# Kernel tuning notes

Measured on AMD Instinct MI355X. Metric: run time of the kernel, lower is better.

The kernel has to match this reference:

```python
import jax, jax.numpy as jnp
import numpy as np

B, T, I, H, O = 512, 1024, 15, 64, 11

def setup_inputs() -> dict:
    key = jax.random.key(0)
    ks = jax.random.split(key, 7)
    s_ih = 1.0 / np.sqrt(H)
    return {
        "x": jax.random.normal(ks[0], (B, T, I), dtype=jnp.float32),
        # torch nn.RNN params: weight_ih_l0 [H,I], weight_hh_l0 [H,H], biases [H]
        "W_ih": jax.random.uniform(ks[1], (H, I), jnp.float32, -s_ih, s_ih),
        "b_ih": jax.random.uniform(ks[2], (H,), jnp.float32, -s_ih, s_ih),
        "W_hh": jax.random.uniform(ks[3], (H, H), jnp.float32, -s_ih, s_ih),
        "b_hh": jax.random.uniform(ks[4], (H,), jnp.float32, -s_ih, s_ih),
        # decoder Linear(64, 11)
        "W_dec": jax.random.uniform(ks[5], (O, H), jnp.float32, -s_ih, s_ih),
        "b_dec": jax.random.uniform(ks[6], (O,), jnp.float32, -s_ih, s_ih),
    }

def reference(x, W_ih, b_ih, W_hh, b_hh, W_dec, b_dec):
    # Precompute input projection for all timesteps: [T, B, H]
    xproj = jnp.einsum("bti,hi->tbh", x, W_ih) + b_ih + b_hh
    h0 = jnp.zeros((x.shape[0], W_hh.shape[0]), dtype=x.dtype)

    def step(h, xp_t):
        h_new = jax.nn.relu(xp_t + h @ W_hh.T)  # [B, H]
        return h_new, h_new

    h_last, hs = jax.lax.scan(step, h0, xproj)  # hs: [T, B, H]
    out_seq = jnp.transpose(hs, (1, 0, 2))       # [B, T, H]
    out = jax.nn.relu(jnp.einsum("bth,oh->bto", out_seq, W_dec) + b_dec)
    h = h_last[None]  # [1, B, H] matching torch num_layers dim
    return (out, h)
```

## Files before the change

kernel.cpp:

```cpp
#include <hip/hip_runtime.h>
#include <hip/hip_fp16.h>
#include <stdint.h>

#define BB 512
#define TT 1024
#define II 15
#define HH 64
#define OO 11

typedef __fp16 half2v __attribute__((ext_vector_type(2)));
typedef float floatx4 __attribute__((ext_vector_type(4)));
typedef int int4v __attribute__((ext_vector_type(4)));

union PK { int i; half2v h; float f; };

__device__ __forceinline__ half2v i2h2(int v) { PK u; u.i = v; return u.h; }
__device__ __forceinline__ int h22i(half2v v) { PK u; u.h = v; return u.i; }

__device__ __forceinline__ float FDOT2(half2v a, half2v b, float c) {
    return __builtin_amdgcn_fdot2(a, b, c, false);
}

__device__ __forceinline__ float lane_xor1(float v) {
    PK u; u.f = v;
    u.i = __builtin_amdgcn_mov_dpp(u.i, 0xB1, 0xF, 0xF, false);
    return u.f;
}

__device__ __forceinline__ float lane_xor2(float v) {
    PK u; u.f = v;
    u.i = __builtin_amdgcn_mov_dpp(u.i, 0x4E, 0xF, 0xF, false);
    return u.f;
}

__device__ __forceinline__ void block_sync() {
    asm volatile("s_waitcnt lgkmcnt(0)" ::: "memory");
    __builtin_amdgcn_s_barrier();
}

__global__ __launch_bounds__(256) void rnn_fused(
    const float* __restrict__ x, const float* __restrict__ W_ih,
    const float* __restrict__ b_ih, const float* __restrict__ W_hh,
    const float* __restrict__ b_hh, const float* __restrict__ W_dec,
    const float* __restrict__ b_dec, float* __restrict__ out,
    float* __restrict__ h_last)
{
    __shared__ __align__(16) int xbuf[2][2][64 * 8];
    __shared__ __align__(16) _Float16 hring[2][128][HH];
    const int tid  = threadIdx.x;
    const int lane = tid & 63;
    const int wid  = tid >> 6;

    if (wid < 2) {
        const int w = wid;
        const int b = blockIdx.x * 2 + w;

        half2v whh[32];
#pragma unroll
        for (int p = 0; p < 32; ++p)
            whh[p] = __builtin_amdgcn_cvt_pkrtz(W_hh[lane * HH + 2 * p],
                                                W_hh[lane * HH + 2 * p + 1]);
        half2v wx[8];
#pragma unroll
        for (int j = 0; j < 7; ++j)
            wx[j] = __builtin_amdgcn_cvt_pkrtz(W_ih[lane * II + 2 * j],
                                               W_ih[lane * II + 2 * j + 1]);
        wx[7] = __builtin_amdgcn_cvt_pkrtz(W_ih[lane * II + 14],
                                           b_ih[lane] + b_hh[lane]);

        const float* xb = x + (size_t)b * TT * II;

        {
            float cf[II];
#pragma unroll
            for (int i = 0; i < II; ++i) cf[i] = xb[lane * II + i];
            int4v p0, p1;
            p0.x = h22i(__builtin_amdgcn_cvt_pkrtz(cf[0], cf[1]));
            p0.y = h22i(__builtin_amdgcn_cvt_pkrtz(cf[2], cf[3]));
            p0.z = h22i(__builtin_amdgcn_cvt_pkrtz(cf[4], cf[5]));
            p0.w = h22i(__builtin_amdgcn_cvt_pkrtz(cf[6], cf[7]));
            p1.x = h22i(__builtin_amdgcn_cvt_pkrtz(cf[8], cf[9]));
            p1.y = h22i(__builtin_amdgcn_cvt_pkrtz(cf[10], cf[11]));
            p1.z = h22i(__builtin_amdgcn_cvt_pkrtz(cf[12], cf[13]));
            p1.w = h22i(__builtin_amdgcn_cvt_pkrtz(cf[14], 1.0f));
            *(int4v*)&xbuf[w][0][lane * 8] = p0;
            *(int4v*)&xbuf[w][0][lane * 8 + 4] = p1;
        }
        hring[w][127][lane] = (_Float16)0.0f;

        float xa[8];
        {
            const int4v xv0 = *(const int4v*)&xbuf[w][0][0];
            const int4v xv1 = *(const int4v*)&xbuf[w][0][4];
            xa[0] = FDOT2(i2h2(xv0.x), wx[0], 0.0f);
            xa[1] = FDOT2(i2h2(xv0.y), wx[1], 0.0f);
            xa[2] = FDOT2(i2h2(xv0.z), wx[2], 0.0f);
            xa[3] = FDOT2(i2h2(xv0.w), wx[3], 0.0f);
            xa[4] = FDOT2(i2h2(xv1.x), wx[4], 0.0f);
            xa[5] = FDOT2(i2h2(xv1.y), wx[5], 0.0f);
            xa[6] = FDOT2(i2h2(xv1.z), wx[6], 0.0f);
            xa[7] = FDOT2(i2h2(xv1.w), wx[7], 0.0f);
        }

        float h = 0.0f;
        int hpk = 0;

        auto step = [&](int t) {
            const int4v* hb4 = (const int4v*)&hring[w][(t + 127) & 127][0];
            int4v hb[6];
#pragma unroll
            for (int q = 0; q < 6; ++q) hb[q] = hb4[q + 2];

            float a0 = xa[0], a1 = xa[1], a2 = xa[2], a3 = xa[3];
            float a4 = xa[4], a5 = xa[5], a6 = xa[6], a7 = xa[7];

            a0 = FDOT2(i2h2(__builtin_amdgcn_readlane(hpk, 0)),  whh[0], a0);
            a1 = FDOT2(i2h2(__builtin_amdgcn_readlane(hpk, 2)),  whh[1], a1);
            a2 = FDOT2(i2h2(__builtin_amdgcn_readlane(hpk, 4)),  whh[2], a2);
            a3 = FDOT2(i2h2(__builtin_amdgcn_readlane(hpk, 6)),  whh[3], a3);
            a4 = FDOT2(i2h2(__builtin_amdgcn_readlane(hpk, 8)),  whh[4], a4);
            a5 = FDOT2(i2h2(__builtin_amdgcn_readlane(hpk, 10)), whh[5], a5);
            a6 = FDOT2(i2h2(__builtin_amdgcn_readlane(hpk, 12)), whh[6], a6);
            a7 = FDOT2(i2h2(__builtin_amdgcn_readlane(hpk, 14)), whh[7], a7);

#pragma unroll
            for (int q = 0; q < 6; ++q) {
                const int base = 8 + 4 * q;
                if ((q & 1) == 0) {
                    a0 = FDOT2(i2h2(hb[q].x), whh[base + 0], a0);
                    a1 = FDOT2(i2h2(hb[q].y), whh[base + 1], a1);
                    a2 = FDOT2(i2h2(hb[q].z), whh[base + 2], a2);
                    a3 = FDOT2(i2h2(hb[q].w), whh[base + 3], a3);
                } else {
                    a4 = FDOT2(i2h2(hb[q].x), whh[base + 0], a4);
                    a5 = FDOT2(i2h2(hb[q].y), whh[base + 1], a5);
                    a6 = FDOT2(i2h2(hb[q].z), whh[base + 2], a6);
                    a7 = FDOT2(i2h2(hb[q].w), whh[base + 3], a7);
                }
            }
            h = fmaxf(((a0 + a1) + (a2 + a3)) + ((a4 + a5) + (a6 + a7)), 0.0f);
            const _Float16 hf = (_Float16)h;
            hring[w][t & 127][lane] = hf;

            const int tn = t + 1;
            const int* xp = &xbuf[w][(tn >> 6) & 1][(tn & 63) * 8];
            const int4v xv0 = *(const int4v*)xp;
            const int4v xv1 = *(const int4v*)(xp + 4);

            hpk = h22i(__builtin_amdgcn_cvt_pkrtz(h, lane_xor1(h)));

            xa[0] = FDOT2(i2h2(xv0.x), wx[0], 0.0f);
            xa[1] = FDOT2(i2h2(xv0.y), wx[1], 0.0f);
            xa[2] = FDOT2(i2h2(xv0.z), wx[2], 0.0f);
            xa[3] = FDOT2(i2h2(xv0.w), wx[3], 0.0f);
            xa[4] = FDOT2(i2h2(xv1.x), wx[4], 0.0f);
            xa[5] = FDOT2(i2h2(xv1.y), wx[5], 0.0f);
            xa[6] = FDOT2(i2h2(xv1.z), wx[6], 0.0f);
            xa[7] = FDOT2(i2h2(xv1.w), wx[7], 0.0f);
        };

        for (int tc = 0; tc < TT; tc += 64) {
            const int tnb = (tc + 64 < TT) ? (tc + 64) : tc;
            float nf[II];
#pragma unroll
            for (int i = 0; i < II; ++i)
                nf[i] = xb[(size_t)(tnb + lane) * II + i];

            for (int to = 0; to < 32; to += 8)
#pragma unroll
                for (int u = 0; u < 8; ++u) step(tc + to + u);

            {
                const int cb = ((tc >> 6) + 1) & 1;
                int4v p0, p1;
                p0.x = h22i(__builtin_amdgcn_cvt_pkrtz(nf[0], nf[1]));
                p0.y = h22i(__builtin_amdgcn_cvt_pkrtz(nf[2], nf[3]));
                p0.z = h22i(__builtin_amdgcn_cvt_pkrtz(nf[4], nf[5]));
                p0.w = h22i(__builtin_amdgcn_cvt_pkrtz(nf[6], nf[7]));
                p1.x = h22i(__builtin_amdgcn_cvt_pkrtz(nf[8], nf[9]));
                p1.y = h22i(__builtin_amdgcn_cvt_pkrtz(nf[10], nf[11]));
                p1.z = h22i(__builtin_amdgcn_cvt_pkrtz(nf[12], nf[13]));
                p1.w = h22i(__builtin_amdgcn_cvt_pkrtz(nf[14], 1.0f));
                *(int4v*)&xbuf[w][cb][lane * 8] = p0;
                *(int4v*)&xbuf[w][cb][lane * 8 + 4] = p1;
            }

            for (int to = 32; to < 64; to += 8)
#pragma unroll
                for (int u = 0; u < 8; ++u) step(tc + to + u);

            block_sync();
        }
        h_last[b * HH + lane] = h;
    } else {
        const int w = wid - 2;
        const int b = blockIdx.x * 2 + w;

        const int od = lane >> 2;
        const int oc = (od < OO) ? od : 0;
        const int ks = lane & 3;
        half2v wdec[8];
#pragma unroll
        for (int p = 0; p < 8; ++p)
            wdec[p] = __builtin_amdgcn_cvt_pkrtz(
                W_dec[oc * HH + (ks * 8 + p) * 2],
                W_dec[oc * HH + (ks * 8 + p) * 2 + 1]);
        const float bd = b_dec[oc];
        const bool dostore = (ks == 0) && (od < OO);
        float* outb = out + (size_t)b * TT * OO + od;

        for (int c = 0; c < TT / 64; ++c) {
            block_sync();
#pragma unroll 4
            for (int lt = 0; lt < 64; ++lt) {
                const int t = c * 64 + lt;
                const char* row = (const char*)&hring[w][t & 127][0];
                const int4v d0 = *(const int4v*)(row + ks * 32);
                const int4v d1 = *(const int4v*)(row + ks * 32 + 16);
                float dacc = FDOT2(i2h2(d0.x), wdec[0], 0.0f);
                dacc = FDOT2(i2h2(d0.y), wdec[1], dacc);
                dacc = FDOT2(i2h2(d0.z), wdec[2], dacc);
                dacc = FDOT2(i2h2(d0.w), wdec[3], dacc);
                dacc = FDOT2(i2h2(d1.x), wdec[4], dacc);
                dacc = FDOT2(i2h2(d1.y), wdec[5], dacc);
                dacc = FDOT2(i2h2(d1.z), wdec[6], dacc);
                dacc = FDOT2(i2h2(d1.w), wdec[7], dacc);
                dacc += lane_xor1(dacc);
                dacc += lane_xor2(dacc);
                if (dostore)
                    outb[(size_t)t * OO] = fmaxf(dacc + bd, 0.0f);
            }
        }
    }
}

extern "C" void kernel_launch(void* const* d_in, const int* in_sizes, int n_in,
                              void* d_out, int out_size, void* d_ws, size_t ws_size,
                              hipStream_t stream) {
    const float* x     = (const float*)d_in[0];
    const float* W_ih  = (const float*)d_in[1];
    const float* b_ih  = (const float*)d_in[2];
    const float* W_hh  = (const float*)d_in[3];
    const float* b_hh  = (const float*)d_in[4];
    const float* W_dec = (const float*)d_in[5];
    const float* b_dec = (const float*)d_in[6];

    float* out    = (float*)d_out;
    float* h_last = out + (size_t)BB * TT * OO;

    rnn_fused<<<BB / 2, 256, 0, stream>>>(x, W_ih, b_ih, W_hh, b_hh,
                                          W_dec, b_dec, out, h_last);
}
```

Baseline: 259.1 us.

## Compute recurrent matvec with MFMA 16x16x32 instead of packed dot2

Replaces the per-lane fdot2 chain over W_hh with eight MFMA 16x16x32 f16 instructions. The hidden vector is broadcast as the A operand, W_hh tiles sit as B fragments in registers, and the needed output element is picked per lane with selects. The goal is to shorten the serial per-timestep latency of the 64x64 matvec. In exchange, most of each MFMA computes redundant rows, and MFMA issue latency plus cross-lane selection sit on the critical recurrence path.

```diff
diff --git a/kernel.cpp b/kernel.cpp
--- a/kernel.cpp
+++ b/kernel.cpp
@@ -9,6 +9,7 @@
 #define OO 11
 
 typedef __fp16 half2v __attribute__((ext_vector_type(2)));
+typedef _Float16 half8 __attribute__((ext_vector_type(8)));
 typedef float floatx4 __attribute__((ext_vector_type(4)));
 typedef int int4v __attribute__((ext_vector_type(4)));
 
@@ -55,11 +56,18 @@
         const int w = wid;
         const int b = blockIdx.x * 2 + w;
 
-        half2v whh[32];
-#pragma unroll
-        for (int p = 0; p < 32; ++p)
-            whh[p] = __builtin_amdgcn_cvt_pkrtz(W_hh[lane * HH + 2 * p],
-                                                W_hh[lane * HH + 2 * p + 1]);
+        const int nl = lane & 15;
+        const int kq = lane >> 4;
+        half8 bf[4][2];
+#pragma unroll
+        for (int g = 0; g < 4; ++g)
+#pragma unroll
+            for (int s = 0; s < 2; ++s)
+#pragma unroll
+                for (int j = 0; j < 8; ++j)
+                    bf[g][s][j] = (_Float16)W_hh[(16 * g + nl) * HH +
+                                                 32 * s + 8 * kq + j];
+
         half2v wx[8];
 #pragma unroll
         for (int j = 0; j < 7; ++j)
@@ -103,51 +111,43 @@
         }
 
         float h = 0.0f;
-        int hpk = 0;
+        const int aoff = kq * 16;
+        const bool b4 = (lane & 16) != 0;
+        const bool b5 = (lane & 32) != 0;
+        const floatx4 zc = {0.0f, 0.0f, 0.0f, 0.0f};
 
         auto step = [&](int t) {
-            const int4v* hb4 = (const int4v*)&hring[w][(t + 127) & 127][0];
-            int4v hb[6];
-#pragma unroll
-            for (int q = 0; q < 6; ++q) hb[q] = hb4[q + 2];
-
-            float a0 = xa[0], a1 = xa[1], a2 = xa[2], a3 = xa[3];
-            float a4 = xa[4], a5 = xa[5], a6 = xa[6], a7 = xa[7];
-
-            a0 = FDOT2(i2h2(__builtin_amdgcn_readlane(hpk, 0)),  whh[0], a0);
-            a1 = FDOT2(i2h2(__builtin_amdgcn_readlane(hpk, 2)),  whh[1], a1);
-            a2 = FDOT2(i2h2(__builtin_amdgcn_readlane(hpk, 4)),  whh[2], a2);
-            a3 = FDOT2(i2h2(__builtin_amdgcn_readlane(hpk, 6)),  whh[3], a3);
-            a4 = FDOT2(i2h2(__builtin_amdgcn_readlane(hpk, 8)),  whh[4], a4);
-            a5 = FDOT2(i2h2(__builtin_amdgcn_readlane(hpk, 10)), whh[5], a5);
-            a6 = FDOT2(i2h2(__builtin_amdgcn_readlane(hpk, 12)), whh[6], a6);
-            a7 = FDOT2(i2h2(__builtin_amdgcn_readlane(hpk, 14)), whh[7], a7);
-
-#pragma unroll
-            for (int q = 0; q < 6; ++q) {
-                const int base = 8 + 4 * q;
-                if ((q & 1) == 0) {
-                    a0 = FDOT2(i2h2(hb[q].x), whh[base + 0], a0);
-                    a1 = FDOT2(i2h2(hb[q].y), whh[base + 1], a1);
-                    a2 = FDOT2(i2h2(hb[q].z), whh[base + 2], a2);
-                    a3 = FDOT2(i2h2(hb[q].w), whh[base + 3], a3);
-                } else {
-                    a4 = FDOT2(i2h2(hb[q].x), whh[base + 0], a4);
-                    a5 = FDOT2(i2h2(hb[q].y), whh[base + 1], a5);
-                    a6 = FDOT2(i2h2(hb[q].z), whh[base + 2], a6);
-                    a7 = FDOT2(i2h2(hb[q].w), whh[base + 3], a7);
-                }
-            }
-            h = fmaxf(((a0 + a1) + (a2 + a3)) + ((a4 + a5) + (a6 + a7)), 0.0f);
-            const _Float16 hf = (_Float16)h;
-            hring[w][t & 127][lane] = hf;
+            const char* hrow = (const char*)&hring[w][(t + 127) & 127][0];
+            const half8 a0 = *(const half8*)(hrow + aoff);
+            const half8 a1 = *(const half8*)(hrow + 64 + aoff);
+
+            const float xs = ((xa[0] + xa[1]) + (xa[2] + xa[3])) +
+                             ((xa[4] + xa[5]) + (xa[6] + xa[7]));
 
             const int tn = t + 1;
             const int* xp = &xbuf[w][(tn >> 6) & 1][(tn & 63) * 8];
             const int4v xv0 = *(const int4v*)xp;
             const int4v xv1 = *(const int4v*)(xp + 4);
 
-            hpk = h22i(__builtin_amdgcn_cvt_pkrtz(h, lane_xor1(h)));
+            floatx4 c0 = __builtin_amdgcn_mfma_f32_16x16x32_f16(a0, bf[0][0], zc, 0, 0, 0);
+            floatx4 d0 = __builtin_amdgcn_mfma_f32_16x16x32_f16(a1, bf[0][1], zc, 0, 0, 0);
+            floatx4 c1 = __builtin_amdgcn_mfma_f32_16x16x32_f16(a0, bf[1][0], zc, 0, 0, 0);
+            floatx4 d1 = __builtin_amdgcn_mfma_f32_16x16x32_f16(a1, bf[1][1], zc, 0, 0, 0);
+            floatx4 c2 = __builtin_amdgcn_mfma_f32_16x16x32_f16(a0, bf[2][0], zc, 0, 0, 0);
+            floatx4 d2 = __builtin_amdgcn_mfma_f32_16x16x32_f16(a1, bf[2][1], zc, 0, 0, 0);
+            floatx4 c3 = __builtin_amdgcn_mfma_f32_16x16x32_f16(a0, bf[3][0], zc, 0, 0, 0);
+            floatx4 d3 = __builtin_amdgcn_mfma_f32_16x16x32_f16(a1, bf[3][1], zc, 0, 0, 0);
+
+            const float v0 = c0[0] + d0[0];
+            const float v1 = c1[0] + d1[0];
+            const float v2 = c2[0] + d2[0];
+            const float v3 = c3[0] + d3[0];
+            const float r01 = b4 ? v1 : v0;
+            const float r23 = b4 ? v3 : v2;
+            const float hpre = b5 ? r23 : r01;
+
+            h = fmaxf(hpre + xs, 0.0f);
+            hring[w][t & 127][lane] = (_Float16)h;
 
             xa[0] = FDOT2(i2h2(xv0.x), wx[0], 0.0f);
             xa[1] = FDOT2(i2h2(xv0.y), wx[1], 0.0f);
```

Measured after the change: 269.3 us. 1.04x slower.

## Move input projection from recurrence waves to decoder waves via LDS staging

Applied to the files above, without the earlier changes.

The input projection x·W_ih + bias is now computed by the decoder wavefronts one chunk ahead and written as fp32 scalars into a double-buffered LDS array. The recurrent wavefronts only read one float per step instead of loading packed x and doing eight extra dot products per step. This takes work off the serial critical path. In exchange it uses much more LDS (64 KB for xsbuf), which may limit occupancy, and it changes the barrier schedule between the two wave groups.

```diff
diff --git a/kernel.cpp b/kernel.cpp
--- a/kernel.cpp
+++ b/kernel.cpp
@@ -7,6 +7,7 @@
 #define II 15
 #define HH 64
 #define OO 11
+#define NC (TT / 64)
 
 typedef __fp16 half2v __attribute__((ext_vector_type(2)));
 typedef float floatx4 __attribute__((ext_vector_type(4)));
@@ -45,21 +46,82 @@
     const float* __restrict__ b_dec, float* __restrict__ out,
     float* __restrict__ h_last)
 {
-    __shared__ __align__(16) int xbuf[2][2][64 * 8];
+    __shared__ __align__(16) int xpack[2][64 * 8];
+    __shared__ __align__(16) float xsbuf[2][2][64 * 64];
     __shared__ __align__(16) _Float16 hring[2][128][HH];
     const int tid  = threadIdx.x;
     const int lane = tid & 63;
     const int wid  = tid >> 6;
+    const int w = wid & 1;
+    const int b = blockIdx.x * 2 + w;
+    const float* xb = x + (size_t)b * TT * II;
 
     if (wid < 2) {
-        const int w = wid;
-        const int b = blockIdx.x * 2 + w;
-
         half2v whh[32];
 #pragma unroll
         for (int p = 0; p < 32; ++p)
             whh[p] = __builtin_amdgcn_cvt_pkrtz(W_hh[lane * HH + 2 * p],
                                                 W_hh[lane * HH + 2 * p + 1]);
+
+        hring[w][127][lane] = (_Float16)0.0f;
+
+        block_sync();
+
+        float h = 0.0f;
+        int hpk = 0;
+
+        for (int c = 0; c < NC; ++c) {
+            const float* xsp = &xsbuf[w][c & 1][0];
+            for (int to = 0; to < 64; to += 8) {
+#pragma unroll
+                for (int u = 0; u < 8; ++u) {
+                    const int ts = to + u;
+                    const int t = c * 64 + ts;
+
+                    const int4v* hb4 =
+                        (const int4v*)&hring[w][(t + 127) & 127][0];
+                    int4v hb[6];
+#pragma unroll
+                    for (int q = 0; q < 6; ++q) hb[q] = hb4[q + 2];
+                    const float xsv = xsp[ts * 64 + lane];
+
+                    float a0, a1, a2, a3, a4, a5, a6, a7;
+                    a0 = FDOT2(i2h2(__builtin_amdgcn_readlane(hpk, 0)),  whh[0], 0.0f);
+                    a1 = FDOT2(i2h2(__builtin_amdgcn_readlane(hpk, 2)),  whh[1], 0.0f);
+                    a2 = FDOT2(i2h2(__builtin_amdgcn_readlane(hpk, 4)),  whh[2], 0.0f);
+                    a3 = FDOT2(i2h2(__builtin_amdgcn_readlane(hpk, 6)),  whh[3], 0.0f);
+                    a4 = FDOT2(i2h2(__builtin_amdgcn_readlane(hpk, 8)),  whh[4], 0.0f);
+                    a5 = FDOT2(i2h2(__builtin_amdgcn_readlane(hpk, 10)), whh[5], 0.0f);
+                    a6 = FDOT2(i2h2(__builtin_amdgcn_readlane(hpk, 12)), whh[6], 0.0f);
+                    a7 = FDOT2(i2h2(__builtin_amdgcn_readlane(hpk, 14)), whh[7], 0.0f);
+
+#pragma unroll
+                    for (int q = 0; q < 6; ++q) {
+                        const int base = 8 + 4 * q;
+                        if ((q & 1) == 0) {
+                            a0 = FDOT2(i2h2(hb[q].x), whh[base + 0], a0);
+                            a1 = FDOT2(i2h2(hb[q].y), whh[base + 1], a1);
+                            a2 = FDOT2(i2h2(hb[q].z), whh[base + 2], a2);
+                            a3 = FDOT2(i2h2(hb[q].w), whh[base + 3], a3);
+                        } else {
+                            a4 = FDOT2(i2h2(hb[q].x), whh[base + 0], a4);
+                            a5 = FDOT2(i2h2(hb[q].y), whh[base + 1], a5);
+                            a6 = FDOT2(i2h2(hb[q].z), whh[base + 2], a6);
+                            a7 = FDOT2(i2h2(hb[q].w), whh[base + 3], a7);
+                        }
+                    }
+                    const float s = ((a0 + a1) + (a2 + a3)) +
+                                    ((a4 + a5) + (a6 + a7));
+                    h = fmaxf(s + xsv, 0.0f);
+                    hring[w][t & 127][lane] = (_Float16)h;
+
+                    hpk = h22i(__builtin_amdgcn_cvt_pkrtz(h, lane_xor1(h)));
+                }
+            }
+            block_sync();
+        }
+        h_last[b * HH + lane] = h;
+    } else {
         half2v wx[8];
 #pragma unroll
         for (int j = 0; j < 7; ++j)
@@ -68,12 +130,24 @@
         wx[7] = __builtin_amdgcn_cvt_pkrtz(W_ih[lane * II + 14],
                                            b_ih[lane] + b_hh[lane]);
 
-        const float* xb = x + (size_t)b * TT * II;
-
-        {
+        const int od = lane >> 2;
+        const int oc = (od < OO) ? od : 0;
+        const int ks = lane & 3;
+        half2v wdec[8];
+#pragma unroll
+        for (int p = 0; p < 8; ++p)
+            wdec[p] = __builtin_amdgcn_cvt_pkrtz(
+                W_dec[oc * HH + (ks * 8 + p) * 2],
+                W_dec[oc * HH + (ks * 8 + p) * 2 + 1]);
+        const float bd = b_dec[oc];
+        const bool dostore = (ks == 0) && (od < OO);
+        float* outb = out + (size_t)b * TT * OO + od;
+
+        auto stage_xs = [&](int chunk) __attribute__((always_inline)) {
+            const float* xc = xb + (size_t)(chunk * 64 + lane) * II;
             float cf[II];
 #pragma unroll
-            for (int i = 0; i < II; ++i) cf[i] = xb[lane * II + i];
+            for (int i = 0; i < II; ++i) cf[i] = xc[i];
             int4v p0, p1;
             p0.x = h22i(__builtin_amdgcn_cvt_pkrtz(cf[0], cf[1]));
             p0.y = h22i(__builtin_amdgcn_cvt_pkrtz(cf[2], cf[3]));
@@ -83,134 +157,29 @@
             p1.y = h22i(__builtin_amdgcn_cvt_pkrtz(cf[10], cf[11]));
             p1.z = h22i(__builtin_amdgcn_cvt_pkrtz(cf[12], cf[13]));
             p1.w = h22i(__builtin_amdgcn_cvt_pkrtz(cf[14], 1.0f));
-            *(int4v*)&xbuf[w][0][lane * 8] = p0;
-            *(int4v*)&xbuf[w][0][lane * 8 + 4] = p1;
-        }
-        hring[w][127][lane] = (_Float16)0.0f;
-
-        float xa[8];
-        {
-            const int4v xv0 = *(const int4v*)&xbuf[w][0][0];
-            const int4v xv1 = *(const int4v*)&xbuf[w][0][4];
-            xa[0] = FDOT2(i2h2(xv0.x), wx[0], 0.0f);
-            xa[1] = FDOT2(i2h2(xv0.y), wx[1], 0.0f);
-            xa[2] = FDOT2(i2h2(xv0.z), wx[2], 0.0f);
-            xa[3] = FDOT2(i2h2(xv0.w), wx[3], 0.0f);
-            xa[4] = FDOT2(i2h2(xv1.x), wx[4], 0.0f);
-            xa[5] = FDOT2(i2h2(xv1.y), wx[5], 0.0f);
-            xa[6] = FDOT2(i2h2(xv1.z), wx[6], 0.0f);
-            xa[7] = FDOT2(i2h2(xv1.w), wx[7], 0.0f);
-        }
-
-        float h = 0.0f;
-        int hpk = 0;
-
-        auto step = [&](int t) {
-            const int4v* hb4 = (const int4v*)&hring[w][(t + 127) & 127][0];
-            int4v hb[6];
-#pragma unroll
-            for (int q = 0; q < 6; ++q) hb[q] = hb4[q + 2];
-
-            float a0 = xa[0], a1 = xa[1], a2 = xa[2], a3 = xa[3];
-            float a4 = xa[4], a5 = xa[5], a6 = xa[6], a7 = xa[7];
-
-            a0 = FDOT2(i2h2(__builtin_amdgcn_readlane(hpk, 0)),  whh[0], a0);
-            a1 = FDOT2(i2h2(__builtin_amdgcn_readlane(hpk, 2)),  whh[1], a1);
-            a2 = FDOT2(i2h2(__builtin_amdgcn_readlane(hpk, 4)),  whh[2], a2);
-            a3 = FDOT2(i2h2(__builtin_amdgcn_readlane(hpk, 6)),  whh[3], a3);
-            a4 = FDOT2(i2h2(__builtin_amdgcn_readlane(hpk, 8)),  whh[4], a4);
-            a5 = FDOT2(i2h2(__builtin_amdgcn_readlane(hpk, 10)), whh[5], a5);
-            a6 = FDOT2(i2h2(__builtin_amdgcn_readlane(hpk, 12)), whh[6], a6);
-            a7 = FDOT2(i2h2(__builtin_amdgcn_readlane(hpk, 14)), whh[7], a7);
-
-#pragma unroll
-            for (int q = 0; q < 6; ++q) {
-                const int base = 8 + 4 * q;
-                if ((q & 1) == 0) {
-                    a0 = FDOT2(i2h2(hb[q].x), whh[base + 0], a0);
-                    a1 = FDOT2(i2h2(hb[q].y), whh[base + 1], a1);
-                    a2 = FDOT2(i2h2(hb[q].z), whh[base + 2], a2);
-                    a3 = FDOT2(i2h2(hb[q].w), whh[base + 3], a3);
-                } else {
-                    a4 = FDOT2(i2h2(hb[q].x), whh[base + 0], a4);
-                    a5 = FDOT2(i2h2(hb[q].y), whh[base + 1], a5);
-                    a6 = FDOT2(i2h2(hb[q].z), whh[base + 2], a6);
-                    a7 = FDOT2(i2h2(hb[q].w), whh[base + 3], a7);
-                }
+            *(int4v*)&xpack[w][lane * 8] = p0;
+            *(int4v*)&xpack[w][lane * 8 + 4] = p1;
+
+            const int4v* xp4 = (const int4v*)&xpack[w][0];
+            float* xsd = &xsbuf[w][chunk & 1][0];
+#pragma unroll 4
+            for (int ts = 0; ts < 64; ++ts) {
+                const int4v xv0 = xp4[2 * ts];
+                const int4v xv1 = xp4[2 * ts + 1];
+                float t0 = FDOT2(i2h2(xv0.x), wx[0], 0.0f);
+                float t1 = FDOT2(i2h2(xv0.y), wx[1], 0.0f);
+                float t2 = FDOT2(i2h2(xv0.z), wx[2], 0.0f);
+                float t3 = FDOT2(i2h2(xv0.w), wx[3], 0.0f);
+                float t4 = FDOT2(i2h2(xv1.x), wx[4], 0.0f);
+                float t5 = FDOT2(i2h2(xv1.y), wx[5], 0.0f);
+                float t6 = FDOT2(i2h2(xv1.z), wx[6], 0.0f);
+                float t7 = FDOT2(i2h2(xv1.w), wx[7], 0.0f);
+                xsd[ts * 64 + lane] = ((t0 + t1) + (t2 + t3)) +
+                                      ((t4 + t5) + (t6 + t7));
             }
-            h = fmaxf(((a0 + a1) + (a2 + a3)) + ((a4 + a5) + (a6 + a7)), 0.0f);
-            const _Float16 hf = (_Float16)h;
-            hring[w][t & 127][lane] = hf;
-
-            const int tn = t + 1;
-            const int* xp = &xbuf[w][(tn >> 6) & 1][(tn & 63) * 8];
-            const int4v xv0 = *(const int4v*)xp;
-            const int4v xv1 = *(const int4v*)(xp + 4);
-
-            hpk = h22i(__builtin_amdgcn_cvt_pkrtz(h, lane_xor1(h)));
-
-            xa[0] = FDOT2(i2h2(xv0.x), wx[0], 0.0f);
-            xa[1] = FDOT2(i2h2(xv0.y), wx[1], 0.0f);
-            xa[2] = FDOT2(i2h2(xv0.z), wx[2], 0.0f);
-            xa[3] = FDOT2(i2h2(xv0.w), wx[3], 0.0f);
-            xa[4] = FDOT2(i2h2(xv1.x), wx[4], 0.0f);
-            xa[5] = FDOT2(i2h2(xv1.y), wx[5], 0.0f);
-            xa[6] = FDOT2(i2h2(xv1.z), wx[6], 0.0f);
-            xa[7] = FDOT2(i2h2(xv1.w), wx[7], 0.0f);
         };
 
-        for (int tc = 0; tc < TT; tc += 64) {
-            const int tnb = (tc + 64 < TT) ? (tc + 64) : tc;
-            float nf[II];
-#pragma unroll
-            for (int i = 0; i < II; ++i)
-                nf[i] = xb[(size_t)(tnb + lane) * II + i];
-
-            for (int to = 0; to < 32; to += 8)
-#pragma unroll
-                for (int u = 0; u < 8; ++u) step(tc + to + u);
-
-            {
-                const int cb = ((tc >> 6) + 1) & 1;
-                int4v p0, p1;
-                p0.x = h22i(__builtin_amdgcn_cvt_pkrtz(nf[0], nf[1]));
-                p0.y = h22i(__builtin_amdgcn_cvt_pkrtz(nf[2], nf[3]));
-                p0.z = h22i(__builtin_amdgcn_cvt_pkrtz(nf[4], nf[5]));
-                p0.w = h22i(__builtin_amdgcn_cvt_pkrtz(nf[6], nf[7]));
-                p1.x = h22i(__builtin_amdgcn_cvt_pkrtz(nf[8], nf[9]));
-                p1.y = h22i(__builtin_amdgcn_cvt_pkrtz(nf[10], nf[11]));
-                p1.z = h22i(__builtin_amdgcn_cvt_pkrtz(nf[12], nf[13]));
-                p1.w = h22i(__builtin_amdgcn_cvt_pkrtz(nf[14], 1.0f));
-                *(int4v*)&xbuf[w][cb][lane * 8] = p0;
-                *(int4v*)&xbuf[w][cb][lane * 8 + 4] = p1;
-            }
-
-            for (int to = 32; to < 64; to += 8)
-#pragma unroll
-                for (int u = 0; u < 8; ++u) step(tc + to + u);
-
-            block_sync();
-        }
-        h_last[b * HH + lane] = h;
-    } else {
-        const int w = wid - 2;
-        const int b = blockIdx.x * 2 + w;
-
-        const int od = lane >> 2;
-        const int oc = (od < OO) ? od : 0;
-        const int ks = lane & 3;
-        half2v wdec[8];
-#pragma unroll
-        for (int p = 0; p < 8; ++p)
-            wdec[p] = __builtin_amdgcn_cvt_pkrtz(
-                W_dec[oc * HH + (ks * 8 + p) * 2],
-                W_dec[oc * HH + (ks * 8 + p) * 2 + 1]);
-        const float bd = b_dec[oc];
-        const bool dostore = (ks == 0) && (od < OO);
-        float* outb = out + (size_t)b * TT * OO + od;
-
-        for (int c = 0; c < TT / 64; ++c) {
-            block_sync();
+        auto decode_chunk = [&](int c) __attribute__((always_inline)) {
 #pragma unroll 4
             for (int lt = 0; lt < 64; ++lt) {
                 const int t = c * 64 + lt;
@@ -230,7 +199,17 @@
                 if (dostore)
                     outb[(size_t)t * OO] = fmaxf(dacc + bd, 0.0f);
             }
+        };
+
+        stage_xs(0);
+        block_sync();
+
+        for (int c = 0; c < NC; ++c) {
+            if (c + 1 < NC) stage_xs(c + 1);
+            if (c >= 1) decode_chunk(c - 1);
+            block_sync();
         }
+        decode_chunk(NC - 1);
     }
 }
 
```

Measured after the change: 246.7 us. -4.8%, faster.
